# Kernel optimization log

Hardware: AMD Instinct MI355X
Metric: run time of the kernel (lower is better)

Reference implementation:

```python
import jax, jax.numpy as jnp
import numpy as np

B, D, P, K = 16384, 2048, 64, 5


def setup_inputs() -> dict:
    key = jax.random.key(0)
    k1, k2, k3, k4, k5 = jax.random.split(key, 5)
    s = 1.0 / np.sqrt(D)
    return {
        "x": jax.random.normal(k1, (B, D), dtype=jnp.float32),
        "parent_W": jax.random.normal(k2, (P, D), dtype=jnp.float32) * s,
        "parent_b": jax.random.normal(k3, (P,), dtype=jnp.float32) * s,
        "child_W": jax.random.normal(k4, (P, K, D), dtype=jnp.float32) * s,
        "child_b": jax.random.normal(k5, (P, K), dtype=jnp.float32) * s,
    }


def reference(x, parent_W, parent_b, child_W, child_b):
    # Parent linear: [B, P]
    parent_logits = x @ parent_W.T + parent_b
    # softmax is monotonic, so argmax(softmax(l)) == argmax(l)
    parent_class = jnp.argmax(parent_logits, axis=1)  # [B] int
    # Gather each sample's expert (child classifier) weights: [B, K, D], [B, K]
    Wc = child_W[parent_class]
    bc = child_b[parent_class]
    # Per-sample tiny GEMM, batched: [B, K]
    child_logits = jnp.einsum("bd,bkd->bk", x, Wc) + bc
    return parent_logits, child_logits
```

## Files before the change

kernel.cpp:

```cpp
#include <hip/hip_runtime.h>

#define B_ 16384
#define D_ 2048
#define P_ 64
#define K_ 5

#define BM 64
#define BK 64
#define NCH (D_ / BK)

__global__ __launch_bounds__(256) void k_parent(
    const float* __restrict__ x, const float* __restrict__ pW,
    const float* __restrict__ pb, float* __restrict__ pout,
    int* __restrict__ pc) {
  __shared__ float smem[BK * BM + BK * P_];
  float* xT = smem;
  float* wT = smem + BK * BM;

  const int tid = threadIdx.x;
  const int b0  = blockIdx.x * BM;
  const int q   = tid & 15;
  const int rw  = tid >> 4;
  const int tc4 = (tid & 15) << 2;
  const int tr4 = (tid >> 4) << 2;

  const float* xg = x + (size_t)b0 * D_;

  float4 xa[4], wb[4];
#pragma unroll
  for (int j = 0; j < 4; ++j) {
    xa[j] = *(const float4*)&xg[(size_t)(rw + 16 * j) * D_ + (q << 2)];
    wb[j] = *(const float4*)&pW[(size_t)(rw + 16 * j) * D_ + (q << 2)];
  }

  float acc[4][4];
#pragma unroll
  for (int i = 0; i < 4; ++i)
#pragma unroll
    for (int jj = 0; jj < 4; ++jj) acc[i][jj] = 0.f;

  const int swz = q << 2;
  for (int kk = 0; kk < NCH; ++kk) {
#pragma unroll
    for (int j = 0; j < 4; ++j) {
      const int cx = (rw + 16 * j) ^ swz;
      xT[(4 * q + 0) * BM + cx] = xa[j].x;
      xT[(4 * q + 1) * BM + cx] = xa[j].y;
      xT[(4 * q + 2) * BM + cx] = xa[j].z;
      xT[(4 * q + 3) * BM + cx] = xa[j].w;
      wT[(4 * q + 0) * P_ + cx] = wb[j].x;
      wT[(4 * q + 1) * P_ + cx] = wb[j].y;
      wT[(4 * q + 2) * P_ + cx] = wb[j].z;
      wT[(4 * q + 3) * P_ + cx] = wb[j].w;
    }
    __syncthreads();
    if (kk + 1 < NCH) {
      const int d0 = (kk + 1) * BK;
#pragma unroll
      for (int j = 0; j < 4; ++j) {
        xa[j] = *(const float4*)&xg[(size_t)(rw + 16 * j) * D_ + d0 + (q << 2)];
        wb[j] = *(const float4*)&pW[(size_t)(rw + 16 * j) * D_ + d0 + (q << 2)];
      }
    }
#pragma unroll 8
    for (int d = 0; d < BK; ++d) {
      const int sz = ((d >> 2) & 15) << 2;
      const float4 xv = *(const float4*)&xT[d * BM + (tr4 ^ sz)];
      const float4 wv = *(const float4*)&wT[d * P_ + (tc4 ^ sz)];
      acc[0][0] += xv.x * wv.x; acc[0][1] += xv.x * wv.y;
      acc[0][2] += xv.x * wv.z; acc[0][3] += xv.x * wv.w;
      acc[1][0] += xv.y * wv.x; acc[1][1] += xv.y * wv.y;
      acc[1][2] += xv.y * wv.z; acc[1][3] += xv.y * wv.w;
      acc[2][0] += xv.z * wv.x; acc[2][1] += xv.z * wv.y;
      acc[2][2] += xv.z * wv.z; acc[2][3] += xv.z * wv.w;
      acc[3][0] += xv.w * wv.x; acc[3][1] += xv.w * wv.y;
      acc[3][2] += xv.w * wv.z; acc[3][3] += xv.w * wv.w;
    }
    __syncthreads();
  }

  const float4 bias = *(const float4*)&pb[tc4];
  float* pl = smem;
#pragma unroll
  for (int ri = 0; ri < 4; ++ri) {
    const int r = tr4 + ri;
    float4 v;
    v.x = acc[ri][0] + bias.x; v.y = acc[ri][1] + bias.y;
    v.z = acc[ri][2] + bias.z; v.w = acc[ri][3] + bias.w;
    *(float4*)&pout[(size_t)(b0 + r) * P_ + tc4] = v;
    *(float4*)&pl[r * 68 + tc4] = v;
  }
  __syncthreads();
  if (tid < BM) {
    const int r = tid;
    float best = pl[r * 68];
    int arg = 0;
#pragma unroll
    for (int p = 1; p < P_; ++p) {
      const float v = pl[r * 68 + p];
      if (v > best) { best = v; arg = p; }
    }
    pc[b0 + r] = arg;
  }
}

__global__ __launch_bounds__(256) void k_child(
    const float* __restrict__ x, const float* __restrict__ cW,
    const float* __restrict__ cb, const int* __restrict__ pc,
    float* __restrict__ cout) {
  __shared__ float wlds[K_ * D_];
  const int e = blockIdx.x >> 4;
  const int m = blockIdx.x & 15;
  const int tid = threadIdx.x;

  const float4* wg4 = (const float4*)(cW + (size_t)e * K_ * D_);
  float4* wl4 = (float4*)wlds;
#pragma unroll
  for (int t = 0; t < 10; ++t) wl4[tid + 256 * t] = wg4[tid + 256 * t];
  __syncthreads();

  const int wave = tid >> 6;
  const int lane = tid & 63;
  const float bk0 = cb[e * K_ + 0], bk1 = cb[e * K_ + 1], bk2 = cb[e * K_ + 2],
              bk3 = cb[e * K_ + 3], bk4 = cb[e * K_ + 4];

  const int rbase0 = m * 1024 + wave * 256;
  for (int it = 0; it < 4; ++it) {
    const int rb = rbase0 + it * 64;
    const int myc = pc[rb + lane];
    unsigned long long mask = __ballot(myc == e);
    while (mask) {
      const int bit = __ffsll(mask) - 1;
      mask &= mask - 1;
      const int r = rb + bit;
      const float4* xr4 = (const float4*)(x + (size_t)r * D_);
      float a0 = 0.f, a1 = 0.f, a2 = 0.f, a3 = 0.f, a4 = 0.f;
#pragma unroll
      for (int t = 0; t < 8; ++t) {
        const float4 xv = xr4[lane + 64 * t];
        const float4 w0 = wl4[lane + 64 * t];
        const float4 w1 = wl4[512 + lane + 64 * t];
        const float4 w2 = wl4[1024 + lane + 64 * t];
        const float4 w3 = wl4[1536 + lane + 64 * t];
        const float4 w4 = wl4[2048 + lane + 64 * t];
        a0 += xv.x * w0.x + xv.y * w0.y + xv.z * w0.z + xv.w * w0.w;
        a1 += xv.x * w1.x + xv.y * w1.y + xv.z * w1.z + xv.w * w1.w;
        a2 += xv.x * w2.x + xv.y * w2.y + xv.z * w2.z + xv.w * w2.w;
        a3 += xv.x * w3.x + xv.y * w3.y + xv.z * w3.z + xv.w * w3.w;
        a4 += xv.x * w4.x + xv.y * w4.y + xv.z * w4.z + xv.w * w4.w;
      }
#pragma unroll
      for (int s = 32; s > 0; s >>= 1) {
        a0 += __shfl_xor(a0, s, 64);
        a1 += __shfl_xor(a1, s, 64);
        a2 += __shfl_xor(a2, s, 64);
        a3 += __shfl_xor(a3, s, 64);
        a4 += __shfl_xor(a4, s, 64);
      }
      if (lane == 0) {
        float* o = cout + (size_t)r * K_;
        o[0] = a0 + bk0; o[1] = a1 + bk1; o[2] = a2 + bk2;
        o[3] = a3 + bk3; o[4] = a4 + bk4;
      }
    }
  }
}

extern "C" void kernel_launch(void* const* d_in, const int* in_sizes, int n_in,
                              void* d_out, int out_size, void* d_ws, size_t ws_size,
                              hipStream_t stream) {
  const float* x  = (const float*)d_in[0];
  const float* pW = (const float*)d_in[1];
  const float* pb = (const float*)d_in[2];
  const float* cW = (const float*)d_in[3];
  const float* cb = (const float*)d_in[4];
  float* pout = (float*)d_out;
  float* cout = (float*)d_out + (size_t)B_ * P_;
  int* pc = (int*)d_ws;

  k_parent<<<B_ / BM, 256, 0, stream>>>(x, pW, pb, pout, pc);
  k_child<<<P_ * 16, 256, 0, stream>>>(x, cW, cb, pc, cout);
}
```

Baseline: 263.1 us.

## Split-K parent GEMM with reduce-argmax bucketing and batched per-expert child pass

The parent linear layer becomes a split-K GEMM. It uses a pre-transposed weight copy and 64-thread blocks that each compute an 8x8 register tile and write partial sums to workspace. A separate reduce kernel adds the partials and bias, takes a wave-level argmax, and appends each row to a per-expert list with atomics. The child kernel then walks only its expert's list and handles four rows per wave iteration, so it no longer scans every row's ballot for every expert. The change adds extra kernels, workspace traffic for the partials, and a fixed 512-slot list per expert that would silently drop rows if one expert gets more than that.

```diff
diff --git a/kernel.cpp b/kernel.cpp
--- a/kernel.cpp
+++ b/kernel.cpp
@@ -5,162 +5,195 @@
 #define P_ 64
 #define K_ 5
 
-#define BM 64
-#define BK 64
-#define NCH (D_ / BK)
-
-__global__ __launch_bounds__(256) void k_parent(
-    const float* __restrict__ x, const float* __restrict__ pW,
-    const float* __restrict__ pb, float* __restrict__ pout,
-    int* __restrict__ pc) {
-  __shared__ float smem[BK * BM + BK * P_];
-  float* xT = smem;
-  float* wT = smem + BK * BM;
-
+__global__ __launch_bounds__(256) void k0_transpose(const float* __restrict__ W,
+                                                    float* __restrict__ wT) {
+  const int i  = blockIdx.x * 256 + threadIdx.x;
+  const int c  = i >> 9;
+  const int d0 = (i & 511) << 2;
+  const float4 v = *(const float4*)&W[c * D_ + d0];
+  wT[(d0 + 0) * P_ + c] = v.x;
+  wT[(d0 + 1) * P_ + c] = v.y;
+  wT[(d0 + 2) * P_ + c] = v.z;
+  wT[(d0 + 3) * P_ + c] = v.w;
+}
+
+__global__ __launch_bounds__(64) void k1_parent(const float* __restrict__ x,
+                                                const float* __restrict__ wT,
+                                                float* __restrict__ part,
+                                                int kslice) {
+  __shared__ float xT[32 * 64];
+  const int t   = threadIdx.x;
+  const int rt  = blockIdx.x & 255;
+  const int ks  = blockIdx.x >> 8;
+  const int b0  = rt * 64;
+  const int kbase = ks * kslice;
+  const int lr8 = (t >> 3) << 3;
+  const int lc8 = (t & 7) << 3;
+
+  const float* xrow = x + (size_t)(b0 + t) * D_ + kbase;
+
+  float4 acc[8][2];
+#pragma unroll
+  for (int i = 0; i < 8; ++i) {
+    acc[i][0] = make_float4(0.f, 0.f, 0.f, 0.f);
+    acc[i][1] = make_float4(0.f, 0.f, 0.f, 0.f);
+  }
+
+  const int nch = kslice >> 5;
+  float4 st[8];
+#pragma unroll
+  for (int j = 0; j < 8; ++j) st[j] = *(const float4*)&xrow[j * 4];
+
+  for (int ch = 0; ch < nch; ++ch) {
+#pragma unroll
+    for (int j = 0; j < 8; ++j) {
+      xT[(4 * j + 0) * 64 + t] = st[j].x;
+      xT[(4 * j + 1) * 64 + t] = st[j].y;
+      xT[(4 * j + 2) * 64 + t] = st[j].z;
+      xT[(4 * j + 3) * 64 + t] = st[j].w;
+    }
+    __syncthreads();
+    if (ch + 1 < nch) {
+      const float* nx = xrow + (ch + 1) * 32;
+#pragma unroll
+      for (int j = 0; j < 8; ++j) st[j] = *(const float4*)&nx[j * 4];
+    }
+    const float* wd = wT + (size_t)(kbase + (ch << 5)) * P_;
+#pragma unroll 4
+    for (int d = 0; d < 32; ++d) {
+      const float4 xv0 = *(const float4*)&xT[d * 64 + lr8];
+      const float4 xv1 = *(const float4*)&xT[d * 64 + lr8 + 4];
+      const float4 wv0 = *(const float4*)&wd[d * 64 + lc8];
+      const float4 wv1 = *(const float4*)&wd[d * 64 + lc8 + 4];
+      const float xs[8] = {xv0.x, xv0.y, xv0.z, xv0.w,
+                           xv1.x, xv1.y, xv1.z, xv1.w};
+#pragma unroll
+      for (int i = 0; i < 8; ++i) {
+        acc[i][0].x += xs[i] * wv0.x; acc[i][0].y += xs[i] * wv0.y;
+        acc[i][0].z += xs[i] * wv0.z; acc[i][0].w += xs[i] * wv0.w;
+        acc[i][1].x += xs[i] * wv1.x; acc[i][1].y += xs[i] * wv1.y;
+        acc[i][1].z += xs[i] * wv1.z; acc[i][1].w += xs[i] * wv1.w;
+      }
+    }
+    __syncthreads();
+  }
+
+  float* po = part + (size_t)ks * (B_ * P_) + (size_t)b0 * P_;
+#pragma unroll
+  for (int i = 0; i < 8; ++i) {
+    *(float4*)&po[(size_t)(lr8 + i) * P_ + lc8]     = acc[i][0];
+    *(float4*)&po[(size_t)(lr8 + i) * P_ + lc8 + 4] = acc[i][1];
+  }
+}
+
+__global__ __launch_bounds__(256) void k_reduce(const float* __restrict__ part,
+                                                const float* __restrict__ pb,
+                                                float* __restrict__ pout,
+                                                int* __restrict__ cnt,
+                                                int* __restrict__ list,
+                                                int KS) {
+  const int wave = threadIdx.x >> 6, lane = threadIdx.x & 63;
+  const int r = blockIdx.x * 4 + wave;
+  float v = pb[lane];
+  for (int s = 0; s < KS; ++s)
+    v += part[(size_t)s * (B_ * P_) + (size_t)r * P_ + lane];
+  pout[(size_t)r * P_ + lane] = v;
+
+  float bv = v;
+  int bi = lane;
+#pragma unroll
+  for (int s = 32; s > 0; s >>= 1) {
+    const float ov = __shfl_xor(bv, s, 64);
+    const int oi = __shfl_xor(bi, s, 64);
+    if (ov > bv || (ov == bv && oi < bi)) { bv = ov; bi = oi; }
+  }
+  if (lane == 0) {
+    const int slot = atomicAdd(&cnt[bi], 1);
+    if (slot < 512) list[bi * 512 + slot] = r;
+  }
+}
+
+__global__ __launch_bounds__(256) void k2_child(const float* __restrict__ x,
+                                                const float* __restrict__ cW,
+                                                const float* __restrict__ cb,
+                                                const int* __restrict__ cnt,
+                                                const int* __restrict__ list,
+                                                float* __restrict__ cout) {
+  __shared__ float wlds[K_ * D_];
+  const int e   = blockIdx.x >> 3;
+  const int chk = blockIdx.x & 7;
   const int tid = threadIdx.x;
-  const int b0  = blockIdx.x * BM;
-  const int q   = tid & 15;
-  const int rw  = tid >> 4;
-  const int tc4 = (tid & 15) << 2;
-  const int tr4 = (tid >> 4) << 2;
-
-  const float* xg = x + (size_t)b0 * D_;
-
-  float4 xa[4], wb[4];
-#pragma unroll
-  for (int j = 0; j < 4; ++j) {
-    xa[j] = *(const float4*)&xg[(size_t)(rw + 16 * j) * D_ + (q << 2)];
-    wb[j] = *(const float4*)&pW[(size_t)(rw + 16 * j) * D_ + (q << 2)];
-  }
-
-  float acc[4][4];
-#pragma unroll
-  for (int i = 0; i < 4; ++i)
-#pragma unroll
-    for (int jj = 0; jj < 4; ++jj) acc[i][jj] = 0.f;
-
-  const int swz = q << 2;
-  for (int kk = 0; kk < NCH; ++kk) {
-#pragma unroll
-    for (int j = 0; j < 4; ++j) {
-      const int cx = (rw + 16 * j) ^ swz;
-      xT[(4 * q + 0) * BM + cx] = xa[j].x;
-      xT[(4 * q + 1) * BM + cx] = xa[j].y;
-      xT[(4 * q + 2) * BM + cx] = xa[j].z;
-      xT[(4 * q + 3) * BM + cx] = xa[j].w;
-      wT[(4 * q + 0) * P_ + cx] = wb[j].x;
-      wT[(4 * q + 1) * P_ + cx] = wb[j].y;
-      wT[(4 * q + 2) * P_ + cx] = wb[j].z;
-      wT[(4 * q + 3) * P_ + cx] = wb[j].w;
-    }
-    __syncthreads();
-    if (kk + 1 < NCH) {
-      const int d0 = (kk + 1) * BK;
-#pragma unroll
-      for (int j = 0; j < 4; ++j) {
-        xa[j] = *(const float4*)&xg[(size_t)(rw + 16 * j) * D_ + d0 + (q << 2)];
-        wb[j] = *(const float4*)&pW[(size_t)(rw + 16 * j) * D_ + d0 + (q << 2)];
+
+  const float4* wg4 = (const float4*)(cW + (size_t)e * (K_ * D_));
+  float4* wl4 = (float4*)wlds;
+#pragma unroll
+  for (int tI = 0; tI < 10; ++tI) wl4[tid + 256 * tI] = wg4[tid + 256 * tI];
+  __syncthreads();
+
+  const int n   = min(cnt[e], 512);
+  const int per = (n + 7) >> 3;
+  const int lo  = chk * per;
+  const int hi  = min(lo + per, n);
+  const int m   = hi - lo;
+  if (m <= 0) return;
+
+  const int wave = tid >> 6, lane = tid & 63;
+  const int wper = (m + 3) >> 2;
+  const int wlo  = lo + wave * wper;
+  const int whi  = min(wlo + wper, hi);
+
+  const float4* x4 = (const float4*)x;
+  const int* mylist = list + e * 512;
+
+  for (int i0 = wlo; i0 < whi; i0 += 4) {
+    const int vb = min(4, whi - i0);
+    const int ra = mylist[i0];
+    const int rb = mylist[i0 + min(1, vb - 1)];
+    const int rc = mylist[i0 + min(2, vb - 1)];
+    const int rd = mylist[i0 + min(3, vb - 1)];
+
+    float a[20];
+#pragma unroll
+    for (int q = 0; q < 20; ++q) a[q] = 0.f;
+
+#pragma unroll
+    for (int tt = 0; tt < 8; ++tt) {
+      const float4 xv0 = x4[(size_t)ra * 512 + lane + 64 * tt];
+      const float4 xv1 = x4[(size_t)rb * 512 + lane + 64 * tt];
+      const float4 xv2 = x4[(size_t)rc * 512 + lane + 64 * tt];
+      const float4 xv3 = x4[(size_t)rd * 512 + lane + 64 * tt];
+#pragma unroll
+      for (int k = 0; k < 5; ++k) {
+        const float4 wv = wl4[k * 512 + lane + 64 * tt];
+        a[0 * 5 + k] += xv0.x * wv.x + xv0.y * wv.y + xv0.z * wv.z + xv0.w * wv.w;
+        a[1 * 5 + k] += xv1.x * wv.x + xv1.y * wv.y + xv1.z * wv.z + xv1.w * wv.w;
+        a[2 * 5 + k] += xv2.x * wv.x + xv2.y * wv.y + xv2.z * wv.z + xv2.w * wv.w;
+        a[3 * 5 + k] += xv3.x * wv.x + xv3.y * wv.y + xv3.z * wv.z + xv3.w * wv.w;
       }
     }
-#pragma unroll 8
-    for (int d = 0; d < BK; ++d) {
-      const int sz = ((d >> 2) & 15) << 2;
-      const float4 xv = *(const float4*)&xT[d * BM + (tr4 ^ sz)];
-      const float4 wv = *(const float4*)&wT[d * P_ + (tc4 ^ sz)];
-      acc[0][0] += xv.x * wv.x; acc[0][1] += xv.x * wv.y;
-      acc[0][2] += xv.x * wv.z; acc[0][3] += xv.x * wv.w;
-      acc[1][0] += xv.y * wv.x; acc[1][1] += xv.y * wv.y;
-      acc[1][2] += xv.y * wv.z; acc[1][3] += xv.y * wv.w;
-      acc[2][0] += xv.z * wv.x; acc[2][1] += xv.z * wv.y;
-      acc[2][2] += xv.z * wv.z; acc[2][3] += xv.z * wv.w;
-      acc[3][0] += xv.w * wv.x; acc[3][1] += xv.w * wv.y;
-      acc[3][2] += xv.w * wv.z; acc[3][3] += xv.w * wv.w;
-    }
-    __syncthreads();
-  }
-
-  const float4 bias = *(const float4*)&pb[tc4];
-  float* pl = smem;
-#pragma unroll
-  for (int ri = 0; ri < 4; ++ri) {
-    const int r = tr4 + ri;
-    float4 v;
-    v.x = acc[ri][0] + bias.x; v.y = acc[ri][1] + bias.y;
-    v.z = acc[ri][2] + bias.z; v.w = acc[ri][3] + bias.w;
-    *(float4*)&pout[(size_t)(b0 + r) * P_ + tc4] = v;
-    *(float4*)&pl[r * 68 + tc4] = v;
-  }
-  __syncthreads();
-  if (tid < BM) {
-    const int r = tid;
-    float best = pl[r * 68];
-    int arg = 0;
-#pragma unroll
-    for (int p = 1; p < P_; ++p) {
-      const float v = pl[r * 68 + p];
-      if (v > best) { best = v; arg = p; }
-    }
-    pc[b0 + r] = arg;
-  }
-}
-
-__global__ __launch_bounds__(256) void k_child(
-    const float* __restrict__ x, const float* __restrict__ cW,
-    const float* __restrict__ cb, const int* __restrict__ pc,
-    float* __restrict__ cout) {
-  __shared__ float wlds[K_ * D_];
-  const int e = blockIdx.x >> 4;
-  const int m = blockIdx.x & 15;
-  const int tid = threadIdx.x;
-
-  const float4* wg4 = (const float4*)(cW + (size_t)e * K_ * D_);
-  float4* wl4 = (float4*)wlds;
-#pragma unroll
-  for (int t = 0; t < 10; ++t) wl4[tid + 256 * t] = wg4[tid + 256 * t];
-  __syncthreads();
-
-  const int wave = tid >> 6;
-  const int lane = tid & 63;
-  const float bk0 = cb[e * K_ + 0], bk1 = cb[e * K_ + 1], bk2 = cb[e * K_ + 2],
-              bk3 = cb[e * K_ + 3], bk4 = cb[e * K_ + 4];
-
-  const int rbase0 = m * 1024 + wave * 256;
-  for (int it = 0; it < 4; ++it) {
-    const int rb = rbase0 + it * 64;
-    const int myc = pc[rb + lane];
-    unsigned long long mask = __ballot(myc == e);
-    while (mask) {
-      const int bit = __ffsll(mask) - 1;
-      mask &= mask - 1;
-      const int r = rb + bit;
-      const float4* xr4 = (const float4*)(x + (size_t)r * D_);
-      float a0 = 0.f, a1 = 0.f, a2 = 0.f, a3 = 0.f, a4 = 0.f;
-#pragma unroll
-      for (int t = 0; t < 8; ++t) {
-        const float4 xv = xr4[lane + 64 * t];
-        const float4 w0 = wl4[lane + 64 * t];
-        const float4 w1 = wl4[512 + lane + 64 * t];
-        const float4 w2 = wl4[1024 + lane + 64 * t];
-        const float4 w3 = wl4[1536 + lane + 64 * t];
-        const float4 w4 = wl4[2048 + lane + 64 * t];
-        a0 += xv.x * w0.x + xv.y * w0.y + xv.z * w0.z + xv.w * w0.w;
-        a1 += xv.x * w1.x + xv.y * w1.y + xv.z * w1.z + xv.w * w1.w;
-        a2 += xv.x * w2.x + xv.y * w2.y + xv.z * w2.z + xv.w * w2.w;
-        a3 += xv.x * w3.x + xv.y * w3.y + xv.z * w3.z + xv.w * w3.w;
-        a4 += xv.x * w4.x + xv.y * w4.y + xv.z * w4.z + xv.w * w4.w;
-      }
-#pragma unroll
-      for (int s = 32; s > 0; s >>= 1) {
-        a0 += __shfl_xor(a0, s, 64);
-        a1 += __shfl_xor(a1, s, 64);
-        a2 += __shfl_xor(a2, s, 64);
-        a3 += __shfl_xor(a3, s, 64);
-        a4 += __shfl_xor(a4, s, 64);
-      }
-      if (lane == 0) {
-        float* o = cout + (size_t)r * K_;
-        o[0] = a0 + bk0; o[1] = a1 + bk1; o[2] = a2 + bk2;
-        o[3] = a3 + bk3; o[4] = a4 + bk4;
+#pragma unroll
+    for (int p = 0; p < 10; ++p) {
+      float va = a[2 * p], vb2 = a[2 * p + 1];
+      va  += __shfl_xor(va, 32, 64);
+      vb2 += __shfl_xor(vb2, 32, 64);
+      float z = (lane < 32) ? va : vb2;
+      z += __shfl_xor(z, 16, 64);
+      z += __shfl_xor(z, 8, 64);
+      z += __shfl_xor(z, 4, 64);
+      z += __shfl_xor(z, 2, 64);
+      z += __shfl_xor(z, 1, 64);
+      a[2 * p] = z;
+    }
+    if (lane == 0 || lane == 32) {
+      const int off = (lane == 32) ? 1 : 0;
+#pragma unroll
+      for (int p = 0; p < 10; ++p) {
+        const int f = 2 * p + off;
+        const int rr = f / 5, kk = f % 5;
+        if (rr < vb) {
+          const int r = (rr == 0) ? ra : (rr == 1) ? rb : (rr == 2) ? rc : rd;
+          cout[(size_t)r * K_ + kk] = a[2 * p] + cb[e * K_ + kk];
+        }
       }
     }
   }
@@ -176,8 +209,28 @@
   const float* cb = (const float*)d_in[4];
   float* pout = (float*)d_out;
   float* cout = (float*)d_out + (size_t)B_ * P_;
-  int* pc = (int*)d_ws;
-
-  k_parent<<<B_ / BM, 256, 0, stream>>>(x, pW, pb, pout, pc);
-  k_child<<<P_ * 16, 256, 0, stream>>>(x, cW, cb, pc, cout);
-}
+
+  char* ws = (char*)d_ws;
+  float* wT   = (float*)ws;
+  int*   cnt  = (int*)(ws + 524288);
+  int*   list = (int*)(ws + 528384);
+  const size_t part_off = 1048576;
+  const size_t part_bytes = (size_t)B_ * P_ * sizeof(float);
+
+  int KS = 1;
+  float* part = pout;
+  for (int cand = 8; cand >= 2; cand >>= 1) {
+    if (part_off + (size_t)cand * part_bytes <= ws_size) {
+      KS = cand;
+      part = (float*)(ws + part_off);
+      break;
+    }
+  }
+  const int kslice = D_ / KS;
+
+  hipMemsetAsync(cnt, 0, 64 * sizeof(int), stream);
+  k0_transpose<<<128, 256, 0, stream>>>(pW, wT);
+  k1_parent<<<256 * KS, 64, 0, stream>>>(x, wT, part, kslice);
+  k_reduce<<<B_ / 4, 256, 0, stream>>>(part, pb, pout, cnt, list, KS);
+  k2_child<<<P_ * 8, 256, 0, stream>>>(x, cW, cb, cnt, list, cout);
+}
```

New measurement: 401.3 us. +52.5%, slower.
